# Optimization experiments

Measured on AMD Instinct MI355X. Metric: run time of the kernel, lower is better.

## Reference

```python
import jax, jax.numpy as jnp
import numpy as np

ALPHA = 0.98
DELTA = 2.0
R = 0.5
EPS = 1e-6


def setup_inputs() -> dict:
    key = jax.random.key(0)
    x = jax.random.uniform(key, (32, 128, 4000), dtype=jnp.float32)
    return {"x": x}


def reference(x):
    # smooth[t] = (1-alpha)*x[t] + alpha*smooth[t-1], smooth[0] = x[0]
    # Expressed as an affine recurrence s_t = A_t * s_{t-1} + B_t and solved
    # with a log-depth associative scan (Blelchoch-style) over the time axis.
    alpha = jnp.asarray(ALPHA, dtype=x.dtype)
    # A: multiplier per step; A[...,0]=0 so s_0 = B_0 = x[...,0]
    A = jnp.full_like(x, alpha).at[..., 0].set(0.0)
    B = jnp.concatenate([x[..., :1], (1.0 - alpha) * x[..., 1:]], axis=-1)

    def combine(c1, c2):
        a1, b1 = c1
        a2, b2 = c2
        return (a2 * a1, a2 * b1 + b2)

    _, smooth = jax.lax.associative_scan(combine, (A, B), axis=-1)

    pcen = (x / (smooth + EPS) ** ALPHA + DELTA) ** R - DELTA ** R
    return pcen
```

## Files before the change

### kernel.cpp

```cpp
#include <hip/hip_runtime.h>
#include <math.h>

#define T_LEN   4000
#define CHUNK   256
#define NCHUNK  16

typedef float v4f __attribute__((ext_vector_type(4)));

__device__ __forceinline__ float pcen_elem(float xv, float s) {
    const float ALPHA = 0.98f;
    const float DELTA = 2.0f;
    const float SQRT_DELTA = 1.4142135623730951f;
    const float EPS = 1e-6f;
    float p = exp2f(-ALPHA * log2f(s + EPS));
    return sqrtf(fmaf(xv, p, DELTA)) - SQRT_DELTA;
}

__global__ __launch_bounds__(256, 4) void pcen_kernel(const float* __restrict__ x,
                                                      float* __restrict__ out,
                                                      int nrows) {
    const float ALPHA = 0.98f;
    const float OMA   = 0.02f;
    const float R1   = 0.92236816f;
    const float R2   = 0.85076302f;
    const float R4   = 0.72379771f;
    const float R8   = 0.52388312f;
    const float R16  = 0.27445352f;
    const float R32  = 0.07532473f;
    const float A256 = 0.00567381f;

    const int lane = threadIdx.x & 63;
    const int wave = threadIdx.x >> 6;
    const int row  = blockIdx.x * 4 + wave;
    if (row >= nrows) return;

    const float* __restrict__ xr   = x   + (size_t)row * T_LEN;
    float* __restrict__       orow = out + (size_t)row * T_LEN;

    float4 v[NCHUNK];
#pragma unroll
    for (int c = 0; c < NCHUNK; ++c) {
        const int t0 = c * CHUNK + lane * 4;
        if (t0 < T_LEN) v[c] = *reinterpret_cast<const float4*>(xr + t0);
        else            v[c] = make_float4(0.f, 0.f, 0.f, 0.f);
    }

    float powl = 1.0f;
    powl *= (lane & 1)  ? R1  : 1.0f;
    powl *= (lane & 2)  ? R2  : 1.0f;
    powl *= (lane & 4)  ? R4  : 1.0f;
    powl *= (lane & 8)  ? R8  : 1.0f;
    powl *= (lane & 16) ? R16 : 1.0f;
    powl *= (lane & 32) ? R32 : 1.0f;

    float s_prev = 0.0f;
#pragma unroll
    for (int c = 0; c < NCHUNK; ++c) {
        const int t0 = c * CHUNK + lane * 4;
        const bool valid = (t0 < T_LEN);
        const float4 vc = v[c];

        float b = (t0 == 0) ? vc.x : OMA * vc.x;
        b = fmaf(ALPHA, b, OMA * vc.y);
        b = fmaf(ALPHA, b, OMA * vc.z);
        b = fmaf(ALPHA, b, OMA * vc.w);

        float bi = b;
        { float bu = __shfl_up(bi, 1);  bi = fmaf(lane >= 1  ? R1  : 0.f, bu, bi); }
        { float bu = __shfl_up(bi, 2);  bi = fmaf(lane >= 2  ? R2  : 0.f, bu, bi); }
        { float bu = __shfl_up(bi, 4);  bi = fmaf(lane >= 4  ? R4  : 0.f, bu, bi); }
        { float bu = __shfl_up(bi, 8);  bi = fmaf(lane >= 8  ? R8  : 0.f, bu, bi); }
        { float bu = __shfl_up(bi, 16); bi = fmaf(lane >= 16 ? R16 : 0.f, bu, bi); }
        { float bu = __shfl_up(bi, 32); bi = fmaf(lane >= 32 ? R32 : 0.f, bu, bi); }

        float be = __shfl_up(bi, 1);
        if (lane == 0) be = 0.0f;
        float s = fmaf(powl, s_prev, be);

        const float b63 = __shfl(bi, 63);
        s_prev = fmaf(A256, s_prev, b63);

        if (valid) {
            float4 o;
            if (t0 == 0) s = vc.x;
            else         s = fmaf(ALPHA, s, OMA * vc.x);
            o.x = pcen_elem(vc.x, s);
            s = fmaf(ALPHA, s, OMA * vc.y);
            o.y = pcen_elem(vc.y, s);
            s = fmaf(ALPHA, s, OMA * vc.z);
            o.z = pcen_elem(vc.z, s);
            s = fmaf(ALPHA, s, OMA * vc.w);
            o.w = pcen_elem(vc.w, s);
            v4f ov = { o.x, o.y, o.z, o.w };
            __builtin_nontemporal_store(ov, reinterpret_cast<v4f*>(orow + t0));
        }
    }
}

extern "C" void kernel_launch(void* const* d_in, const int* in_sizes, int n_in,
                              void* d_out, int out_size, void* d_ws, size_t ws_size,
                              hipStream_t stream) {
    const float* x = (const float*)d_in[0];
    float* out = (float*)d_out;
    const int nrows = in_sizes[0] / T_LEN;
    const int rows_per_block = 4;
    const int grid = (nrows + rows_per_block - 1) / rows_per_block;
    pcen_kernel<<<grid, 256, 0, stream>>>(x, out, nrows);
}
```

Measured before the change: 114.9 us.

## Split each row's scan across two waves using a truncated lookback carry

Each row is now handled by two wavefronts, one per half of the time axis, which doubles the number of independent waves. The second-half wave rebuilds its starting smoothing state by scanning the 512 samples just before the midpoint, relying on the decay of alpha^512 to make the ignored earlier history negligible. Inputs are now loaded per chunk instead of all being preloaded into registers, launch bounds are raised to target more resident waves, and stores switch from nontemporal to plain. The lookback adds redundant scan work and a small approximation error in the second half of each row.

```diff
diff --git a/kernel.cpp b/kernel.cpp
--- a/kernel.cpp
+++ b/kernel.cpp
@@ -2,10 +2,10 @@
 #include <math.h>
 
 #define T_LEN   4000
+#define HALF    2000
 #define CHUNK   256
-#define NCHUNK  16
-
-typedef float v4f __attribute__((ext_vector_type(4)));
+#define NCHUNK  8
+#define LB      2
 
 __device__ __forceinline__ float pcen_elem(float xv, float s) {
     const float ALPHA = 0.98f;
@@ -16,34 +16,29 @@
     return sqrtf(fmaf(xv, p, DELTA)) - SQRT_DELTA;
 }
 
-__global__ __launch_bounds__(256, 4) void pcen_kernel(const float* __restrict__ x,
+__global__ __launch_bounds__(256, 6) void pcen_kernel(const float* __restrict__ x,
                                                       float* __restrict__ out,
                                                       int nrows) {
     const float ALPHA = 0.98f;
     const float OMA   = 0.02f;
     const float R1   = 0.92236816f;
     const float R2   = 0.85076302f;
-    const float R4   = 0.72379771f;
-    const float R8   = 0.52388312f;
-    const float R16  = 0.27445352f;
-    const float R32  = 0.07532473f;
-    const float A256 = 0.00567381f;
+    const float R4   = 0.72379773f;
+    const float R8   = 0.52388316f;
+    const float R16  = 0.27445340f;
+    const float R32  = 0.07532467f;
+    const float A256 = 0.00567380f;
 
     const int lane = threadIdx.x & 63;
     const int wave = threadIdx.x >> 6;
-    const int row  = blockIdx.x * 4 + wave;
+    const int wid  = blockIdx.x * 4 + wave;
+    const int row  = wid >> 1;
+    const int half = wid & 1;
     if (row >= nrows) return;
 
     const float* __restrict__ xr   = x   + (size_t)row * T_LEN;
     float* __restrict__       orow = out + (size_t)row * T_LEN;
-
-    float4 v[NCHUNK];
-#pragma unroll
-    for (int c = 0; c < NCHUNK; ++c) {
-        const int t0 = c * CHUNK + lane * 4;
-        if (t0 < T_LEN) v[c] = *reinterpret_cast<const float4*>(xr + t0);
-        else            v[c] = make_float4(0.f, 0.f, 0.f, 0.f);
-    }
+    const int base = half * HALF;
 
     float powl = 1.0f;
     powl *= (lane & 1)  ? R1  : 1.0f;
@@ -54,11 +49,34 @@
     powl *= (lane & 32) ? R32 : 1.0f;
 
     float s_prev = 0.0f;
+    if (half == 1) {
+#pragma unroll
+        for (int lb = 0; lb < LB; ++lb) {
+            const int t0 = HALF - LB * CHUNK + lb * CHUNK + lane * 4;
+            const float4 vc = *reinterpret_cast<const float4*>(xr + t0);
+            float b = OMA * vc.x;
+            b = fmaf(ALPHA, b, OMA * vc.y);
+            b = fmaf(ALPHA, b, OMA * vc.z);
+            b = fmaf(ALPHA, b, OMA * vc.w);
+            float bi = b;
+            { float bu = __shfl_up(bi, 1);  bi = fmaf(lane >= 1  ? R1  : 0.f, bu, bi); }
+            { float bu = __shfl_up(bi, 2);  bi = fmaf(lane >= 2  ? R2  : 0.f, bu, bi); }
+            { float bu = __shfl_up(bi, 4);  bi = fmaf(lane >= 4  ? R4  : 0.f, bu, bi); }
+            { float bu = __shfl_up(bi, 8);  bi = fmaf(lane >= 8  ? R8  : 0.f, bu, bi); }
+            { float bu = __shfl_up(bi, 16); bi = fmaf(lane >= 16 ? R16 : 0.f, bu, bi); }
+            { float bu = __shfl_up(bi, 32); bi = fmaf(lane >= 32 ? R32 : 0.f, bu, bi); }
+            const float b63 = __shfl(bi, 63);
+            s_prev = fmaf(A256, s_prev, b63);
+        }
+    }
+
 #pragma unroll
     for (int c = 0; c < NCHUNK; ++c) {
-        const int t0 = c * CHUNK + lane * 4;
-        const bool valid = (t0 < T_LEN);
-        const float4 vc = v[c];
+        const int t0 = base + c * CHUNK + lane * 4;
+        const bool valid = (t0 < base + HALF);
+
+        float4 vc = make_float4(0.f, 0.f, 0.f, 0.f);
+        if (valid) vc = *reinterpret_cast<const float4*>(xr + t0);
 
         float b = (t0 == 0) ? vc.x : OMA * vc.x;
         b = fmaf(ALPHA, b, OMA * vc.y);
@@ -91,8 +109,7 @@
             o.z = pcen_elem(vc.z, s);
             s = fmaf(ALPHA, s, OMA * vc.w);
             o.w = pcen_elem(vc.w, s);
-            v4f ov = { o.x, o.y, o.z, o.w };
-            __builtin_nontemporal_store(ov, reinterpret_cast<v4f*>(orow + t0));
+            *reinterpret_cast<float4*>(orow + t0) = o;
         }
     }
 }
@@ -103,7 +120,7 @@
     const float* x = (const float*)d_in[0];
     float* out = (float*)d_out;
     const int nrows = in_sizes[0] / T_LEN;
-    const int rows_per_block = 4;
-    const int grid = (nrows + rows_per_block - 1) / rows_per_block;
+    const int nwaves = nrows * 2;
+    const int grid = (nwaves + 3) / 4;
     pcen_kernel<<<grid, 256, 0, stream>>>(x, out, nrows);
 }
```

New measurement: 113.3 us. Within noise of the previous version (-1.4%).

## Split each row across waves with truncated look-back carry recomputation

Applied to the files above, without the earlier changes.

Each wave now processes a single 256-element chunk instead of looping over all 16 chunks of a row, and it recomputes the incoming scan carry from only the two preceding chunks, since alpha^512 is negligible. This multiplies the number of independent waves to expose far more parallelism and memory-level concurrency than the serial per-row loop. The cost is up to three times the global loads (mostly L2 hits) and redundant scans, plus a small truncation error in the carry. Launch bounds change and the nontemporal store becomes a plain store.

```diff
diff --git a/kernel.cpp b/kernel.cpp
--- a/kernel.cpp
+++ b/kernel.cpp
@@ -4,8 +4,6 @@
 #define T_LEN   4000
 #define CHUNK   256
 #define NCHUNK  16
-
-typedef float v4f __attribute__((ext_vector_type(4)));
 
 __device__ __forceinline__ float pcen_elem(float xv, float s) {
     const float ALPHA = 0.98f;
@@ -16,34 +14,65 @@
     return sqrtf(fmaf(xv, p, DELTA)) - SQRT_DELTA;
 }
 
-__global__ __launch_bounds__(256, 4) void pcen_kernel(const float* __restrict__ x,
+__device__ __forceinline__ float compose4(float4 v, bool is_t0) {
+    const float ALPHA = 0.98f;
+    const float OMA   = 0.02f;
+    float b = is_t0 ? v.x : OMA * v.x;
+    b = fmaf(ALPHA, b, OMA * v.y);
+    b = fmaf(ALPHA, b, OMA * v.z);
+    b = fmaf(ALPHA, b, OMA * v.w);
+    return b;
+}
+
+__device__ __forceinline__ float ks_scan(float b, int lane) {
+    const float R1  = 0.92236816f;
+    const float R2  = 0.85076302f;
+    const float R4  = 0.72379773f;
+    const float R8  = 0.52388316f;
+    const float R16 = 0.27445340f;
+    const float R32 = 0.07532467f;
+    float bi = b;
+    { float bu = __shfl_up(bi, 1);  bi = fmaf(lane >= 1  ? R1  : 0.f, bu, bi); }
+    { float bu = __shfl_up(bi, 2);  bi = fmaf(lane >= 2  ? R2  : 0.f, bu, bi); }
+    { float bu = __shfl_up(bi, 4);  bi = fmaf(lane >= 4  ? R4  : 0.f, bu, bi); }
+    { float bu = __shfl_up(bi, 8);  bi = fmaf(lane >= 8  ? R8  : 0.f, bu, bi); }
+    { float bu = __shfl_up(bi, 16); bi = fmaf(lane >= 16 ? R16 : 0.f, bu, bi); }
+    { float bu = __shfl_up(bi, 32); bi = fmaf(lane >= 32 ? R32 : 0.f, bu, bi); }
+    return bi;
+}
+
+__global__ __launch_bounds__(256, 6) void pcen_kernel(const float* __restrict__ x,
                                                       float* __restrict__ out,
                                                       int nrows) {
     const float ALPHA = 0.98f;
     const float OMA   = 0.02f;
     const float R1   = 0.92236816f;
     const float R2   = 0.85076302f;
-    const float R4   = 0.72379771f;
-    const float R8   = 0.52388312f;
-    const float R16  = 0.27445352f;
-    const float R32  = 0.07532473f;
-    const float A256 = 0.00567381f;
+    const float R4   = 0.72379773f;
+    const float R8   = 0.52388316f;
+    const float R16  = 0.27445340f;
+    const float R32  = 0.07532467f;
+    const float A256 = 0.00567380f;
 
     const int lane = threadIdx.x & 63;
     const int wave = threadIdx.x >> 6;
-    const int row  = blockIdx.x * 4 + wave;
+    const int row  = blockIdx.x >> 2;
+    const int cq   = (blockIdx.x & 3) * 4 + wave;
     if (row >= nrows) return;
 
     const float* __restrict__ xr   = x   + (size_t)row * T_LEN;
     float* __restrict__       orow = out + (size_t)row * T_LEN;
 
-    float4 v[NCHUNK];
-#pragma unroll
-    for (int c = 0; c < NCHUNK; ++c) {
-        const int t0 = c * CHUNK + lane * 4;
-        if (t0 < T_LEN) v[c] = *reinterpret_cast<const float4*>(xr + t0);
-        else            v[c] = make_float4(0.f, 0.f, 0.f, 0.f);
-    }
+    const int nlb = (cq < 2) ? cq : 2;
+    const int c0  = cq - nlb;
+    float4 vl0 = make_float4(0.f, 0.f, 0.f, 0.f);
+    float4 vl1 = make_float4(0.f, 0.f, 0.f, 0.f);
+    if (nlb > 0) vl0 = *reinterpret_cast<const float4*>(xr + c0 * CHUNK + lane * 4);
+    if (nlb > 1) vl1 = *reinterpret_cast<const float4*>(xr + (c0 + 1) * CHUNK + lane * 4);
+    const int t_main = cq * CHUNK + lane * 4;
+    const bool valid = (t_main < T_LEN);
+    float4 vm = make_float4(0.f, 0.f, 0.f, 0.f);
+    if (valid) vm = *reinterpret_cast<const float4*>(xr + t_main);
 
     float powl = 1.0f;
     powl *= (lane & 1)  ? R1  : 1.0f;
@@ -54,46 +83,36 @@
     powl *= (lane & 32) ? R32 : 1.0f;
 
     float s_prev = 0.0f;
-#pragma unroll
-    for (int c = 0; c < NCHUNK; ++c) {
-        const int t0 = c * CHUNK + lane * 4;
-        const bool valid = (t0 < T_LEN);
-        const float4 vc = v[c];
+    if (nlb > 0) {
+        const float b0  = compose4(vl0, (c0 == 0) && (lane == 0));
+        const float bi0 = ks_scan(b0, lane);
+        s_prev = __shfl(bi0, 63);
+        if (nlb > 1) {
+            const float b1  = compose4(vl1, false);
+            const float bi1 = ks_scan(b1, lane);
+            s_prev = fmaf(A256, s_prev, __shfl(bi1, 63));
+        }
+    }
 
-        float b = (t0 == 0) ? vc.x : OMA * vc.x;
-        b = fmaf(ALPHA, b, OMA * vc.y);
-        b = fmaf(ALPHA, b, OMA * vc.z);
-        b = fmaf(ALPHA, b, OMA * vc.w);
+    const float bm  = compose4(vm, (cq == 0) && (lane == 0));
+    const float bim = ks_scan(bm, lane);
 
-        float bi = b;
-        { float bu = __shfl_up(bi, 1);  bi = fmaf(lane >= 1  ? R1  : 0.f, bu, bi); }
-        { float bu = __shfl_up(bi, 2);  bi = fmaf(lane >= 2  ? R2  : 0.f, bu, bi); }
-        { float bu = __shfl_up(bi, 4);  bi = fmaf(lane >= 4  ? R4  : 0.f, bu, bi); }
-        { float bu = __shfl_up(bi, 8);  bi = fmaf(lane >= 8  ? R8  : 0.f, bu, bi); }
-        { float bu = __shfl_up(bi, 16); bi = fmaf(lane >= 16 ? R16 : 0.f, bu, bi); }
-        { float bu = __shfl_up(bi, 32); bi = fmaf(lane >= 32 ? R32 : 0.f, bu, bi); }
+    float be = __shfl_up(bim, 1);
+    if (lane == 0) be = 0.0f;
+    float s = fmaf(powl, s_prev, be);
 
-        float be = __shfl_up(bi, 1);
-        if (lane == 0) be = 0.0f;
-        float s = fmaf(powl, s_prev, be);
-
-        const float b63 = __shfl(bi, 63);
-        s_prev = fmaf(A256, s_prev, b63);
-
-        if (valid) {
-            float4 o;
-            if (t0 == 0) s = vc.x;
-            else         s = fmaf(ALPHA, s, OMA * vc.x);
-            o.x = pcen_elem(vc.x, s);
-            s = fmaf(ALPHA, s, OMA * vc.y);
-            o.y = pcen_elem(vc.y, s);
-            s = fmaf(ALPHA, s, OMA * vc.z);
-            o.z = pcen_elem(vc.z, s);
-            s = fmaf(ALPHA, s, OMA * vc.w);
-            o.w = pcen_elem(vc.w, s);
-            v4f ov = { o.x, o.y, o.z, o.w };
-            __builtin_nontemporal_store(ov, reinterpret_cast<v4f*>(orow + t0));
-        }
+    if (valid) {
+        float4 o;
+        if (t_main == 0) s = vm.x;
+        else             s = fmaf(ALPHA, s, OMA * vm.x);
+        o.x = pcen_elem(vm.x, s);
+        s = fmaf(ALPHA, s, OMA * vm.y);
+        o.y = pcen_elem(vm.y, s);
+        s = fmaf(ALPHA, s, OMA * vm.z);
+        o.z = pcen_elem(vm.z, s);
+        s = fmaf(ALPHA, s, OMA * vm.w);
+        o.w = pcen_elem(vm.w, s);
+        *reinterpret_cast<float4*>(orow + t_main) = o;
     }
 }
 
@@ -103,7 +122,6 @@
     const float* x = (const float*)d_in[0];
     float* out = (float*)d_out;
     const int nrows = in_sizes[0] / T_LEN;
-    const int rows_per_block = 4;
-    const int grid = (nrows + rows_per_block - 1) / rows_per_block;
+    const int grid  = nrows * 4;
     pcen_kernel<<<grid, 256, 0, stream>>>(x, out, nrows);
 }
```

Measured after the change: 121.9 us. 1.06x slower.
